# Kernel tuning notes

Hardware: AMD Instinct MI355X
Metric: run time of the kernel (lower is better)

The kernel has to match this reference:

```python
import jax, jax.numpy as jnp
import numpy as np
import math

# ---- hyperparameters (from __init__) ----
S = 64.0
M = 0.45
EASY_MARGIN = False
ALPHA = 0.0
BETA = 0.0
EPS_OT = 0.1   # self.eps
NITER = 6      # self.niter
COS_M = math.cos(M)
SIN_M = math.sin(M)
TH = math.cos(math.pi - M)
MM = math.sin(math.pi - M) * M

# ---- shapes ----
B = 24
D_EMB = 512
N_CLASSES = 10000
C_CH = 256   # channels -> number of OT points per image
H = 14       # spatial -> point dim H*H = 196


def setup_inputs() -> dict:
    key = jax.random.key(0)
    k1, k2, k3, k4 = jax.random.split(key, 4)
    embeddings = jax.random.normal(k1, (B, D_EMB), dtype=jnp.float32)
    conv_features = jax.random.normal(k2, (B, C_CH, H, H), dtype=jnp.float32)
    label = jax.random.randint(k3, (B,), 0, 8)
    # nn.init.normal_(kernel, std=0.01)
    kernel = jax.random.normal(k4, (D_EMB, N_CLASSES), dtype=jnp.float32) * 0.01
    return {"embeddings": embeddings, "conv_features": conv_features,
            "kernel": kernel, "label": label, "epoch": 1}


def _cdist(x, y):
    # Euclidean pairwise distance via GEMM: x (n,d), y (m,d) -> (n,m)
    x2 = jnp.sum(x * x, axis=-1)[:, None]
    y2 = jnp.sum(y * y, axis=-1)[None, :]
    d2 = jnp.maximum(x2 + y2 - 2.0 * (x @ y.T), 0.0)
    return jnp.sqrt(d2 + 1e-12)


def _sinkhorn_dist(x, y):
    # Entropic OT distance <T, C> with uniform marginals, log-domain Sinkhorn.
    C = _cdist(x, y)                       # (n, m)
    n, m = C.shape
    log_mu = -jnp.log(jnp.float32(n))
    log_nu = -jnp.log(jnp.float32(m))
    f = jnp.zeros((n,), C.dtype)
    g = jnp.zeros((m,), C.dtype)
    for _ in range(NITER):  # fixed 6 iterations
        f = -EPS_OT * jax.nn.logsumexp((g[None, :] - C) / EPS_OT + log_nu, axis=1)
        g = -EPS_OT * jax.nn.logsumexp((f[:, None] - C) / EPS_OT + log_mu, axis=0)
    T = jnp.exp((f[:, None] + g[None, :] - C) / EPS_OT + log_mu + log_nu)
    return jnp.sum(T * C)


def reference(embeddings, conv_features, kernel, label, epoch):
    b = embeddings.shape[0]
    emb = embeddings / jnp.linalg.norm(embeddings, axis=1, keepdims=True)
    kn = kernel / jnp.linalg.norm(kernel, axis=0, keepdims=True)
    cos_theta = jnp.clip(emb @ kn, -1.0, 1.0)          # (B, n_classes)
    origin_cos = cos_theta

    rows = jnp.arange(b)
    tl = cos_theta[rows, label]                         # target logit (B,)
    sin_t = jnp.sqrt(jnp.maximum(1.0 - tl * tl, 0.0))
    ctm = tl * COS_M - sin_t * SIN_M
    if EASY_MARGIN:
        ftl = jnp.where(tl > 0.0, ctm, tl)
    else:
        ftl = jnp.where(tl > TH, ctm, tl - MM)
    cos_theta = cos_theta.at[rows, label].set(ftl)
    arcfaceloss = cos_theta * S

    # ---- triplet mining on embedding cosine similarities ----
    dists = emb @ emb.T                                 # (B, B) cosine sims
    eq = label[:, None] == label[None, :]               # (B, B) same-class mask
    # diff_low[a,p,n] = cos(a,n) - cos(a,p)
    diff = dists[:, None, :] - dists[:, :, None]        # (a, p, n)
    valid = eq[:, :, None] & (~eq)[:, None, :] & (diff > -ALPHA)
    n_cosine_pair = jnp.sum(valid)

    if epoch >= 0:
        feats = conv_features.reshape(b, conv_features.shape[1], -1)  # (B, C, H*H)
        # batched Sinkhorn distance for all (a,b) image pairs: (B, B)
        D = jax.vmap(lambda xa: jax.vmap(lambda xb: _sinkhorn_dist(xa, xb))(feats))(feats)
        dis = jnp.maximum(D[:, :, None] - D[:, None, :], -BETA)       # (a, p, n)
        hit = valid & (dis > 0.0)
        ot_pair = jnp.sum(hit)
        wass = jnp.sum(jnp.where(hit, dis, 0.0))
        wass_loss = jnp.where(wass > 0.0,
                              wass / jnp.maximum(ot_pair, 1).astype(wass.dtype),
                              jnp.zeros((), wass.dtype))
    else:
        ot_pair = jnp.zeros((), jnp.int32)
        wass_loss = jnp.zeros(())

    return (arcfaceloss, wass_loss, origin_cos * S, n_cosine_pair, ot_pair)
```

## Files before the change

### kernel.cpp

```cpp
#include <hip/hip_runtime.h>
#include <math.h>

#define B_SZ 24
#define D_EMBD 512
#define N_CLS 10000
#define CC 256
#define HH 196
#define KPAD 224

#define NPAIR 276
#define NARC 40
#define NGRAM 36

#define S_SCALE 64.0f
#define COS_M 0.9004471023526769f
#define SIN_M 0.43496553411123023f
#define TH_C (-0.9004471023526769f)
#define MM_C 0.19573449035005357f
#define KSC 14.4269504088896f
#define C2E 0.0693147180559945f

typedef short bfrag8 __attribute__((ext_vector_type(8)));
typedef float facc4 __attribute__((ext_vector_type(4)));

#if __has_builtin(__builtin_amdgcn_exp2f)
#define EXP2F(x) __builtin_amdgcn_exp2f(x)
#else
#define EXP2F(x) exp2f(x)
#endif
#if __has_builtin(__builtin_amdgcn_logf)
#define LOG2F(x) __builtin_amdgcn_logf(x)
#else
#define LOG2F(x) __log2f(x)
#endif

__device__ inline unsigned short f2bf_rne(float x) {
    union { float f; unsigned u; } cv; cv.f = x;
    unsigned r = cv.u + 0x7FFFu + ((cv.u >> 16) & 1u);
    return (unsigned short)(r >> 16);
}
__device__ inline float bf2f(unsigned short h) {
    union { unsigned u; float f; } cv; cv.u = ((unsigned)h) << 16; return cv.f;
}

__global__ __launch_bounds__(1024) void k_pre(const float* __restrict__ conv,
        unsigned short* __restrict__ hiP, unsigned short* __restrict__ loP,
        float* __restrict__ nrm) {
    const int t = threadIdx.x;
    const int img = blockIdx.x;
    const int row = t >> 2, sch = t & 3;
    const float* src = conv + (img*CC + row)*HH;
    unsigned short* hb = hiP + (img*CC + row)*KPAD;
    unsigned short* lb = loP + (img*CC + row)*KPAD;
    float ps = 0.f;
    for (int c = sch; c < 28; c += 4) {
        const int k0 = c*8;
        float v[8];
        if (k0 + 8 <= HH) {
            const float4* s4 = (const float4*)(src + k0);
            float4 u0 = s4[0], u1 = s4[1];
            v[0]=u0.x; v[1]=u0.y; v[2]=u0.z; v[3]=u0.w;
            v[4]=u1.x; v[5]=u1.y; v[6]=u1.z; v[7]=u1.w;
        } else {
            #pragma unroll
            for (int j = 0; j < 8; ++j) v[j] = (k0 + j < HH) ? src[k0 + j] : 0.f;
        }
        union { unsigned short s[8]; bfrag8 v8; } uh, ul;
        #pragma unroll
        for (int j = 0; j < 8; ++j) {
            ps = fmaf(v[j], v[j], ps);
            unsigned short hbv = f2bf_rne(v[j]);
            uh.s[j] = hbv;
            ul.s[j] = f2bf_rne(v[j] - bf2f(hbv));
        }
        *(bfrag8*)(hb + k0) = uh.v8;
        *(bfrag8*)(lb + k0) = ul.v8;
    }
    ps += __shfl_xor(ps, 1, 64); ps += __shfl_xor(ps, 2, 64);
    if (sch == 0) nrm[img*CC + row] = ps;
}

__global__ __launch_bounds__(1024) void k_fused_pre(const float* __restrict__ emb,
        const float* __restrict__ kern, const int* __restrict__ label,
        const unsigned short* __restrict__ hiP, const unsigned short* __restrict__ loP,
        const float* __restrict__ nrm, float* __restrict__ dists,
        float* __restrict__ Dmat, float* __restrict__ out) {
    const int t = threadIdx.x;
    const int bid = blockIdx.x;

    __shared__ __align__(16) char smem[131072];

    if (bid >= NPAIR) {
        const int sb = bid - NPAIR;
        if (sb >= NARC) {
            const int gid = sb - NARC;
            int l = t & 63, w16 = t >> 6;
            if (gid == 0 && t < B_SZ) Dmat[t * B_SZ + t] = 0.f;
            int pid = gid * 16 + w16;
            if (pid >= B_SZ * B_SZ) return;
            int i = pid / B_SZ, j = pid - (pid / B_SZ) * B_SZ;
            float sij = 0.f, sii = 0.f, sjj = 0.f;
            #pragma unroll
            for (int u = 0; u < 8; ++u) {
                float vi = emb[i*D_EMBD + u*64 + l];
                float vj = emb[j*D_EMBD + u*64 + l];
                sij = fmaf(vi, vj, sij); sii = fmaf(vi, vi, sii); sjj = fmaf(vj, vj, sjj);
            }
            #pragma unroll
            for (int o = 1; o < 64; o <<= 1) {
                sij += __shfl_xor(sij, o, 64);
                sii += __shfl_xor(sii, o, 64);
                sjj += __shfl_xor(sjj, o, 64);
            }
            if (l == 0) dists[pid] = sij * rsqrtf(sii * sjj);
            return;
        }

        float* es = (float*)smem;
        float* inv_s = es + B_SZ * D_EMBD;
        int* lab_s = (int*)(inv_s + B_SZ);
        {
            const float4* s4 = (const float4*)emb;
            float4* d4 = (float4*)es;
            #pragma unroll
            for (int i = 0; i < 3; ++i) d4[i*1024 + t] = s4[i*1024 + t];
        }
        if (t < B_SZ) lab_s[t] = label[t];
        __syncthreads();
        {
            int l = t & 63, w = t >> 6;
            for (int r = w; r < B_SZ; r += 16) {
                float s = 0.f;
                #pragma unroll
                for (int u = 0; u < 8; ++u) { float v = es[r*D_EMBD + u*64 + l]; s = fmaf(v, v, s); }
                #pragma unroll
                for (int o = 1; o < 64; o <<= 1) s += __shfl_xor(s, o, 64);
                if (l == 0) inv_s[r] = rsqrtf(s);
            }
        }
        __syncthreads();

        const int cc = t >> 2, kc = t & 3;
        const int col = sb * 256 + cc;
        const int cL = col < N_CLS ? col : N_CLS - 1;
        float acc[B_SZ];
        #pragma unroll
        for (int r = 0; r < B_SZ; ++r) acc[r] = 0.f;
        float cn = 0.f;
        const int kb0 = kc << 7;
        for (int u = 0; u < 32; ++u) {
            const int um = (u + kc) & 31;
            const int kb = kb0 + (um << 2);
            float kv0 = kern[(kb+0)*N_CLS + cL];
            float kv1 = kern[(kb+1)*N_CLS + cL];
            float kv2 = kern[(kb+2)*N_CLS + cL];
            float kv3 = kern[(kb+3)*N_CLS + cL];
            cn = fmaf(kv0,kv0,cn); cn = fmaf(kv1,kv1,cn);
            cn = fmaf(kv2,kv2,cn); cn = fmaf(kv3,kv3,cn);
            #pragma unroll
            for (int r = 0; r < B_SZ; ++r) {
                const float4 e = *(const float4*)&es[r*D_EMBD + kb];
                acc[r] = fmaf(e.x, kv0, acc[r]);
                acc[r] = fmaf(e.y, kv1, acc[r]);
                acc[r] = fmaf(e.z, kv2, acc[r]);
                acc[r] = fmaf(e.w, kv3, acc[r]);
            }
        }
        cn += __shfl_xor(cn, 1, 64); cn += __shfl_xor(cn, 2, 64);
        #pragma unroll
        for (int r = 0; r < B_SZ; ++r) {
            acc[r] += __shfl_xor(acc[r], 1, 64);
            acc[r] += __shfl_xor(acc[r], 2, 64);
        }
        if (kc == 0 && col < N_CLS) {
            const float invk = rsqrtf(cn);
            #pragma unroll
            for (int r = 0; r < B_SZ; ++r) {
                float cosv = fminf(fmaxf(acc[r] * inv_s[r] * invk, -1.f), 1.f);
                float oc = cosv * S_SCALE;
                float af = oc;
                if (lab_s[r] == col) {
                    float tl = cosv;
                    float sint = sqrtf(fmaxf(1.f - tl*tl, 0.f));
                    float ctm = tl*COS_M - sint*SIN_M;
                    float ftl = (tl > TH_C) ? ctm : (tl - MM_C);
                    af = ftl * S_SCALE;
                }
                out[r*N_CLS + col] = af;
                out[240001 + r*N_CLS + col] = oc;
            }
        }
        return;
    }

    unsigned short* SB = (unsigned short*)smem;
    float* rowred = (float*)smem;
    float* colred = rowred + 1024;
    float* rm_l   = colred + 1024;
    float* z_l    = rm_l + 256;
    float* g_l    = z_l + 256;
    float* q_l    = g_l + 256;
    float* p_l    = q_l + 256;
    float* na_s   = p_l + 256;
    float* nb_s   = na_s + 256;
    float* wredF  = nb_s + 256;
    float* wredG  = wredF + 4;
    float* wredD  = wredG + 4;
    float* gsh    = wredD + 16;

    const int w = t >> 6;
    const int wr = w >> 2, wc = w & 3;
    const int q = (t >> 4) & 3, c0 = t & 15;
    const int R0 = wr * 64, C0 = wc * 64;

    int rem = bid, a = 0;
    while (rem >= 23 - a) { rem -= 23 - a; ++a; }
    int b = a + 1 + rem;

    const int sn = t >> 2;
    const int sch = t & 3;
    const unsigned short* gAh = hiP + (a*CC + sn)*KPAD + sch*8;
    const unsigned short* gAl = loP + (a*CC + sn)*KPAD + sch*8;
    const unsigned short* gBh = hiP + (b*CC + sn)*KPAD + sch*8;
    const unsigned short* gBl = loP + (b*CC + sn)*KPAD + sch*8;
    const int so = sn*32 + sch*8;

    facc4 acc[4][4];
    #pragma unroll
    for (int i = 0; i < 4; ++i)
        #pragma unroll
        for (int j = 0; j < 4; ++j) acc[i][j] = (facc4){0.f, 0.f, 0.f, 0.f};

    uint4 pAh, pAl, pBh, pBl;
    pAh = *(const uint4*)(gAh); pAl = *(const uint4*)(gAl);
    pBh = *(const uint4*)(gBh); pBl = *(const uint4*)(gBl);
    {
        unsigned short* base = SB;
        *(uint4*)(base + so)          = pAh;
        *(uint4*)(base + 8192 + so)   = pAl;
        *(uint4*)(base + 16384 + so)  = pBh;
        *(uint4*)(base + 24576 + so)  = pBl;
    }
    pAh = *(const uint4*)(gAh + 32); pAl = *(const uint4*)(gAl + 32);
    pBh = *(const uint4*)(gBh + 32); pBl = *(const uint4*)(gBl + 32);

    for (int s = 0; s < 7; ++s) {
        __syncthreads();
        if (s < 6) {
            unsigned short* base = SB + ((s + 1) & 1) * 32768;
            *(uint4*)(base + so)          = pAh;
            *(uint4*)(base + 8192 + so)   = pAl;
            *(uint4*)(base + 16384 + so)  = pBh;
            *(uint4*)(base + 24576 + so)  = pBl;
        }
        unsigned short* Ah = SB + (s & 1) * 32768;
        unsigned short* Al = Ah + 8192;
        unsigned short* Bh = Al + 8192;
        unsigned short* Bl = Bh + 8192;
        bfrag8 bh4[4], bl4[4];
        #pragma unroll
        for (int tj = 0; tj < 4; ++tj) {
            int col = C0 + tj*16 + c0;
            bh4[tj] = *(const bfrag8*)(Bh + col*32 + q*8);
            bl4[tj] = *(const bfrag8*)(Bl + col*32 + q*8);
        }
        #pragma unroll
        for (int ti = 0; ti < 4; ++ti) {
            int row = R0 + ti*16 + c0;
            bfrag8 ah = *(const bfrag8*)(Ah + row*32 + q*8);
            bfrag8 al = *(const bfrag8*)(Al + row*32 + q*8);
            #pragma unroll
            for (int tj = 0; tj < 4; ++tj) {
                acc[ti][tj] = __builtin_amdgcn_mfma_f32_16x16x32_bf16(ah, bh4[tj], acc[ti][tj], 0, 0, 0);
                acc[ti][tj] = __builtin_amdgcn_mfma_f32_16x16x32_bf16(ah, bl4[tj], acc[ti][tj], 0, 0, 0);
                acc[ti][tj] = __builtin_amdgcn_mfma_f32_16x16x32_bf16(al, bh4[tj], acc[ti][tj], 0, 0, 0);
            }
        }
        if (s < 5) {
            const int ko = (s + 2) * 32;
            pAh = *(const uint4*)(gAh + ko); pAl = *(const uint4*)(gAl + ko);
            pBh = *(const uint4*)(gBh + ko); pBl = *(const uint4*)(gBl + ko);
        }
    }
    __syncthreads();

    if (t < 256) {
        na_s[t] = nrm[a*CC + t];
        nb_s[t] = nrm[b*CC + t];
        p_l[t] = 1.f;
    }
    if (t < 4) { wredG[t] = 0.f; wredF[t] = 8.f; }
    if (t == 0) *gsh = 0.f;
    __syncthreads();

    facc4 E[4][4];
    {
        float nbv[4];
        #pragma unroll
        for (int tj = 0; tj < 4; ++tj) nbv[tj] = nb_s[C0 + tj*16 + c0];
        #pragma unroll
        for (int ti = 0; ti < 4; ++ti) {
            facc4 nav = *(const facc4*)&na_s[R0 + ti*16 + q*4];
            #pragma unroll
            for (int tj = 0; tj < 4; ++tj) {
                #pragma unroll
                for (int r = 0; r < 4; ++r) {
                    float d2 = fmaxf(nav[r] + nbv[tj] - 2.f*acc[ti][tj][r], 0.f);
                    E[ti][tj][r] = KSC * sqrtf(d2 + 1e-12f);
                }
            }
        }
    }

    const int istar = ((c0&1)<<3) | ((c0&2)<<1) | ((c0&4)>>1) | ((c0&8)>>3);
    const int rowstar = R0 + (istar>>2)*16 + q*4 + (istar&3);
    const int tjstar = ((q&1)<<1) | (q>>1);
    const int colstar = C0 + tjstar*16 + c0;

    {
        float v16[16];
        #pragma unroll
        for (int ti = 0; ti < 4; ++ti)
            #pragma unroll
            for (int r = 0; r < 4; ++r)
                v16[ti*4+r] = fminf(fminf(E[ti][0][r], E[ti][1][r]),
                                    fminf(E[ti][2][r], E[ti][3][r]));
        #pragma unroll
        for (int p = 0; p < 4; ++p) {
            const int m = 1 << p, hsz = 8 >> p;
            const bool hi = (c0 >> p) & 1;
            #pragma unroll
            for (int j = 0; j < hsz; ++j) {
                float mine = hi ? v16[j+hsz] : v16[j];
                float send = hi ? v16[j] : v16[j+hsz];
                v16[j] = fminf(mine, __shfl_xor(send, m, 64));
            }
        }
        rowred[wc*256 + rowstar] = v16[0];
    }
    __syncthreads();
    if (t < 256)
        rm_l[t] = fminf(fminf(rowred[t], rowred[256+t]), fminf(rowred[512+t], rowred[768+t]));
    __syncthreads();

    #pragma unroll
    for (int ti = 0; ti < 4; ++ti) {
        facc4 rmv = *(const facc4*)&rm_l[R0 + ti*16 + q*4];
        #pragma unroll
        for (int tj = 0; tj < 4; ++tj)
            #pragma unroll
            for (int r = 0; r < 4; ++r)
                E[ti][tj][r] = EXP2F(rmv[r] - E[ti][tj][r]);
    }

    #pragma unroll 1
    for (int it = 0; it < 6; ++it) {
        float Gstale = fmaxf(fmaxf(wredG[0], wredG[1]), fmaxf(wredG[2], wredG[3]));
        float MS     = fmaxf(fmaxf(wredF[0], wredF[1]), fmaxf(wredF[2], wredF[3]));
        float P4[4];
        #pragma unroll
        for (int tj = 0; tj < 4; ++tj) P4[tj] = p_l[C0 + tj*16 + c0];
        float v16[16];
        #pragma unroll
        for (int ti = 0; ti < 4; ++ti)
            #pragma unroll
            for (int r = 0; r < 4; ++r) {
                float s = 0.f;
                #pragma unroll
                for (int tj = 0; tj < 4; ++tj) s = fmaf(E[ti][tj][r], P4[tj], s);
                v16[ti*4+r] = s;
            }
        #pragma unroll
        for (int p = 0; p < 4; ++p) {
            const int m = 1 << p, hsz = 8 >> p;
            const bool hi = (c0 >> p) & 1;
            #pragma unroll
            for (int j = 0; j < hsz; ++j) {
                float mine = hi ? v16[j+hsz] : v16[j];
                float send = hi ? v16[j] : v16[j+hsz];
                v16[j] = mine + __shfl_xor(send, m, 64);
            }
        }
        rowred[wc*256 + rowstar] = v16[0];
        __syncthreads();
        if (t < 256) {
            float GS = *gsh;
            float s = rowred[t] + rowred[256+t] + rowred[512+t] + rowred[768+t];
            float z = 8.f - GS - LOG2F(s);
            z_l[t] = z;
            q_l[t] = EXP2F(z - MS);
            float m = z;
            #pragma unroll
            for (int o = 1; o < 64; o <<= 1) m = fmaxf(m, __shfl_xor(m, o, 64));
            if ((t & 63) == 0) wredF[t >> 6] = m;
        }
        __syncthreads();
        float Q[16];
        #pragma unroll
        for (int ti = 0; ti < 4; ++ti) {
            facc4 qv = *(const facc4*)&q_l[R0 + ti*16 + q*4];
            #pragma unroll
            for (int r = 0; r < 4; ++r) Q[ti*4+r] = qv[r];
        }
        float w4[4];
        #pragma unroll
        for (int tj = 0; tj < 4; ++tj) {
            float s = 0.f;
            #pragma unroll
            for (int ti = 0; ti < 4; ++ti)
                #pragma unroll
                for (int r = 0; r < 4; ++r) s = fmaf(E[ti][tj][r], Q[ti*4+r], s);
            w4[tj] = s;
        }
        #pragma unroll
        for (int p = 0; p < 2; ++p) {
            const int m = 16 << p, hsz = 2 >> p;
            const bool hi = (q >> p) & 1;
            #pragma unroll
            for (int j = 0; j < hsz; ++j) {
                float mine = hi ? w4[j+hsz] : w4[j];
                float send = hi ? w4[j] : w4[j+hsz];
                w4[j] = mine + __shfl_xor(send, m, 64);
            }
        }
        colred[wr*256 + colstar] = w4[0];
        __syncthreads();
        if (t < 256) {
            float s = colred[t] + colred[256+t] + colred[512+t] + colred[768+t];
            float G = 8.f - MS - LOG2F(s);
            g_l[t] = G;
            p_l[t] = EXP2F(G - Gstale);
            float m = G;
            #pragma unroll
            for (int o = 1; o < 64; o <<= 1) m = fmaxf(m, __shfl_xor(m, o, 64));
            if ((t & 63) == 0) wredG[t >> 6] = m;
            if (t == 0) *gsh = Gstale;
        }
        __syncthreads();
    }

    {
        float G4[4];
        #pragma unroll
        for (int tj = 0; tj < 4; ++tj) G4[tj] = g_l[C0 + tj*16 + c0] - 16.f;
        float d = 0.f;
        #pragma unroll
        for (int ti = 0; ti < 4; ++ti) {
            facc4 zv = *(const facc4*)&z_l[R0 + ti*16 + q*4];
            facc4 rmv = *(const facc4*)&rm_l[R0 + ti*16 + q*4];
            #pragma unroll
            for (int tj = 0; tj < 4; ++tj) {
                #pragma unroll
                for (int r = 0; r < 4; ++r) {
                    float e = fmaxf(E[ti][tj][r], 1e-45f);
                    float lE = LOG2F(e);
                    float ce = rmv[r] - lE;
                    d = fmaf(EXP2F(zv[r] + G4[tj] + lE), ce, d);
                }
            }
        }
        d *= C2E;
        #pragma unroll
        for (int o = 1; o < 64; o <<= 1) d += __shfl_xor(d, o, 64);
        if ((t & 63) == 0) wredD[w] = d;
        __syncthreads();
        if (t == 0) {
            float s = 0.f;
            #pragma unroll
            for (int i = 0; i < 16; ++i) s += wredD[i];
            Dmat[a*B_SZ + b] = s;
            Dmat[b*B_SZ + a] = s;
        }
    }
}

__global__ __launch_bounds__(1024) void k_fused_loc(const float* __restrict__ emb,
        const float* __restrict__ conv, const float* __restrict__ kern,
        const int* __restrict__ label, float* __restrict__ dists,
        float* __restrict__ Dmat, float* __restrict__ out) {
    const int t = threadIdx.x;
    const int bid = blockIdx.x;

    __shared__ __align__(16) char smem[65536];

    if (bid >= NPAIR) {
        const int sb = bid - NPAIR;
        if (sb >= NARC) {
            const int gid = sb - NARC;
            int l = t & 63, w16 = t >> 6;
            if (gid == 0 && t < B_SZ) Dmat[t * B_SZ + t] = 0.f;
            int pid = gid * 16 + w16;
            if (pid >= B_SZ * B_SZ) return;
            int i = pid / B_SZ, j = pid - (pid / B_SZ) * B_SZ;
            float sij = 0.f, sii = 0.f, sjj = 0.f;
            #pragma unroll
            for (int u = 0; u < 8; ++u) {
                float vi = emb[i*D_EMBD + u*64 + l];
                float vj = emb[j*D_EMBD + u*64 + l];
                sij = fmaf(vi, vj, sij); sii = fmaf(vi, vi, sii); sjj = fmaf(vj, vj, sjj);
            }
            #pragma unroll
            for (int o = 1; o < 64; o <<= 1) {
                sij += __shfl_xor(sij, o, 64);
                sii += __shfl_xor(sii, o, 64);
                sjj += __shfl_xor(sjj, o, 64);
            }
            if (l == 0) dists[pid] = sij * rsqrtf(sii * sjj);
            return;
        }

        float* es = (float*)smem;
        float* inv_s = es + B_SZ * D_EMBD;
        int* lab_s = (int*)(inv_s + B_SZ);
        {
            const float4* s4 = (const float4*)emb;
            float4* d4 = (float4*)es;
            #pragma unroll
            for (int i = 0; i < 3; ++i) d4[i*1024 + t] = s4[i*1024 + t];
        }
        if (t < B_SZ) lab_s[t] = label[t];
        __syncthreads();
        {
            int l = t & 63, w = t >> 6;
            for (int r = w; r < B_SZ; r += 16) {
                float s = 0.f;
                #pragma unroll
                for (int u = 0; u < 8; ++u) { float v = es[r*D_EMBD + u*64 + l]; s = fmaf(v, v, s); }
                #pragma unroll
                for (int o = 1; o < 64; o <<= 1) s += __shfl_xor(s, o, 64);
                if (l == 0) inv_s[r] = rsqrtf(s);
            }
        }
        __syncthreads();

        const int cc = t >> 2, kc = t & 3;
        const int col = sb * 256 + cc;
        const int cL = col < N_CLS ? col : N_CLS - 1;
        float acc[B_SZ];
        #pragma unroll
        for (int r = 0; r < B_SZ; ++r) acc[r] = 0.f;
        float cn = 0.f;
        const int kb0 = kc << 7;
        for (int u = 0; u < 32; ++u) {
            const int um = (u + kc) & 31;
            const int kb = kb0 + (um << 2);
            float kv0 = kern[(kb+0)*N_CLS + cL];
            float kv1 = kern[(kb+1)*N_CLS + cL];
            float kv2 = kern[(kb+2)*N_CLS + cL];
            float kv3 = kern[(kb+3)*N_CLS + cL];
            cn = fmaf(kv0,kv0,cn); cn = fmaf(kv1,kv1,cn);
            cn = fmaf(kv2,kv2,cn); cn = fmaf(kv3,kv3,cn);
            #pragma unroll
            for (int r = 0; r < B_SZ; ++r) {
                const float4 e = *(const float4*)&es[r*D_EMBD + kb];
                acc[r] = fmaf(e.x, kv0, acc[r]);
                acc[r] = fmaf(e.y, kv1, acc[r]);
                acc[r] = fmaf(e.z, kv2, acc[r]);
                acc[r] = fmaf(e.w, kv3, acc[r]);
            }
        }
        cn += __shfl_xor(cn, 1, 64); cn += __shfl_xor(cn, 2, 64);
        #pragma unroll
        for (int r = 0; r < B_SZ; ++r) {
            acc[r] += __shfl_xor(acc[r], 1, 64);
            acc[r] += __shfl_xor(acc[r], 2, 64);
        }
        if (kc == 0 && col < N_CLS) {
            const float invk = rsqrtf(cn);
            #pragma unroll
            for (int r = 0; r < B_SZ; ++r) {
                float cosv = fminf(fmaxf(acc[r] * inv_s[r] * invk, -1.f), 1.f);
                float oc = cosv * S_SCALE;
                float af = oc;
                if (lab_s[r] == col) {
                    float tl = cosv;
                    float sint = sqrtf(fmaxf(1.f - tl*tl, 0.f));
                    float ctm = tl*COS_M - sint*SIN_M;
                    float ftl = (tl > TH_C) ? ctm : (tl - MM_C);
                    af = ftl * S_SCALE;
                }
                out[r*N_CLS + col] = af;
                out[240001 + r*N_CLS + col] = oc;
            }
        }
        return;
    }

    unsigned short* Ah = (unsigned short*)smem;
    unsigned short* Al = Ah + 8192;
    unsigned short* Bh = Al + 8192;
    unsigned short* Bl = Bh + 8192;
    float* rowred = (float*)smem;
    float* colred = rowred + 1024;
    float* rm_l   = colred + 1024;
    float* z_l    = rm_l + 256;
    float* g_l    = z_l + 256;
    float* q_l    = g_l + 256;
    float* p_l    = q_l + 256;
    float* na_s   = p_l + 256;
    float* nb_s   = na_s + 256;
    float* wredF  = nb_s + 256;
    float* wredG  = wredF + 4;
    float* wredD  = wredG + 4;
    float* gsh    = wredD + 16;

    const int w = t >> 6;
    const int wr = w >> 2, wc = w & 3;
    const int q = (t >> 4) & 3, c0 = t & 15;
    const int R0 = wr * 64, C0 = wc * 64;

    int rem = bid, a = 0;
    while (rem >= 23 - a) { rem -= 23 - a; ++a; }
    int b = a + 1 + rem;
    const float* xa = conv + a*CC*HH;
    const float* xb = conv + b*CC*HH;

    const int sn = t >> 2;
    const int sch = t & 3;

    facc4 acc[4][4];
    #pragma unroll
    for (int i = 0; i < 4; ++i)
        #pragma unroll
        for (int j = 0; j < 4; ++j) acc[i][j] = (facc4){0.f, 0.f, 0.f, 0.f};

    float pa = 0.f, pb = 0.f;

    for (int ks = 0; ks < 224; ks += 32) {
        __syncthreads();
        #pragma unroll
        for (int p = 0; p < 2; ++p) {
            int k0 = ks + sch*8;
            const float* src = (p ? xb : xa) + sn*HH + k0;
            float v[8];
            if (k0 + 8 <= HH) {
                const float4* s4 = (const float4*)src;
                float4 u0 = s4[0], u1 = s4[1];
                v[0]=u0.x; v[1]=u0.y; v[2]=u0.z; v[3]=u0.w;
                v[4]=u1.x; v[5]=u1.y; v[6]=u1.z; v[7]=u1.w;
            } else {
                #pragma unroll
                for (int j = 0; j < 8; ++j) v[j] = (k0 + j < HH) ? src[j] : 0.f;
            }
            float ps = 0.f;
            union { unsigned short s[8]; bfrag8 v8; } uh, ul;
            #pragma unroll
            for (int j = 0; j < 8; ++j) {
                ps = fmaf(v[j], v[j], ps);
                unsigned short hb = f2bf_rne(v[j]);
                uh.s[j] = hb;
                ul.s[j] = f2bf_rne(v[j] - bf2f(hb));
            }
            if (p) pb += ps; else pa += ps;
            unsigned short* dh = (p ? Bh : Ah) + sn*32 + sch*8;
            unsigned short* dl = (p ? Bl : Al) + sn*32 + sch*8;
            *(bfrag8*)dh = uh.v8;
            *(bfrag8*)dl = ul.v8;
        }
        __syncthreads();
        bfrag8 bh4[4], bl4[4];
        #pragma unroll
        for (int tj = 0; tj < 4; ++tj) {
            int col = C0 + tj*16 + c0;
            bh4[tj] = *(const bfrag8*)(Bh + col*32 + q*8);
            bl4[tj] = *(const bfrag8*)(Bl + col*32 + q*8);
        }
        #pragma unroll
        for (int ti = 0; ti < 4; ++ti) {
            int row = R0 + ti*16 + c0;
            bfrag8 ah = *(const bfrag8*)(Ah + row*32 + q*8);
            bfrag8 al = *(const bfrag8*)(Al + row*32 + q*8);
            #pragma unroll
            for (int tj = 0; tj < 4; ++tj) {
                acc[ti][tj] = __builtin_amdgcn_mfma_f32_16x16x32_bf16(ah, bh4[tj], acc[ti][tj], 0, 0, 0);
                acc[ti][tj] = __builtin_amdgcn_mfma_f32_16x16x32_bf16(ah, bl4[tj], acc[ti][tj], 0, 0, 0);
                acc[ti][tj] = __builtin_amdgcn_mfma_f32_16x16x32_bf16(al, bh4[tj], acc[ti][tj], 0, 0, 0);
            }
        }
    }
    __syncthreads();

    pa += __shfl_xor(pa, 1, 64); pa += __shfl_xor(pa, 2, 64);
    pb += __shfl_xor(pb, 1, 64); pb += __shfl_xor(pb, 2, 64);
    if (sch == 0) { na_s[sn] = pa; nb_s[sn] = pb; }
    if (t < 256) p_l[t] = 1.f;
    if (t < 4) { wredG[t] = 0.f; wredF[t] = 8.f; }
    if (t == 0) *gsh = 0.f;
    __syncthreads();

    facc4 E[4][4];
    {
        float nbv[4];
        #pragma unroll
        for (int tj = 0; tj < 4; ++tj) nbv[tj] = nb_s[C0 + tj*16 + c0];
        #pragma unroll
        for (int ti = 0; ti < 4; ++ti) {
            facc4 nav = *(const facc4*)&na_s[R0 + ti*16 + q*4];
            #pragma unroll
            for (int tj = 0; tj < 4; ++tj) {
                #pragma unroll
                for (int r = 0; r < 4; ++r) {
                    float d2 = fmaxf(nav[r] + nbv[tj] - 2.f*acc[ti][tj][r], 0.f);
                    E[ti][tj][r] = KSC * sqrtf(d2 + 1e-12f);
                }
            }
        }
    }

    const int istar = ((c0&1)<<3) | ((c0&2)<<1) | ((c0&4)>>1) | ((c0&8)>>3);
    const int rowstar = R0 + (istar>>2)*16 + q*4 + (istar&3);
    const int tjstar = ((q&1)<<1) | (q>>1);
    const int colstar = C0 + tjstar*16 + c0;

    {
        float v16[16];
        #pragma unroll
        for (int ti = 0; ti < 4; ++ti)
            #pragma unroll
            for (int r = 0; r < 4; ++r)
                v16[ti*4+r] = fminf(fminf(E[ti][0][r], E[ti][1][r]),
                                    fminf(E[ti][2][r], E[ti][3][r]));
        #pragma unroll
        for (int p = 0; p < 4; ++p) {
            const int m = 1 << p, hsz = 8 >> p;
            const bool hi = (c0 >> p) & 1;
            #pragma unroll
            for (int j = 0; j < hsz; ++j) {
                float mine = hi ? v16[j+hsz] : v16[j];
                float send = hi ? v16[j] : v16[j+hsz];
                v16[j] = fminf(mine, __shfl_xor(send, m, 64));
            }
        }
        rowred[wc*256 + rowstar] = v16[0];
    }
    __syncthreads();
    if (t < 256)
        rm_l[t] = fminf(fminf(rowred[t], rowred[256+t]), fminf(rowred[512+t], rowred[768+t]));
    __syncthreads();

    #pragma unroll
    for (int ti = 0; ti < 4; ++ti) {
        facc4 rmv = *(const facc4*)&rm_l[R0 + ti*16 + q*4];
        #pragma unroll
        for (int tj = 0; tj < 4; ++tj)
            #pragma unroll
            for (int r = 0; r < 4; ++r)
                E[ti][tj][r] = EXP2F(rmv[r] - E[ti][tj][r]);
    }

    #pragma unroll 1
    for (int it = 0; it < 6; ++it) {
        float Gstale = fmaxf(fmaxf(wredG[0], wredG[1]), fmaxf(wredG[2], wredG[3]));
        float MS     = fmaxf(fmaxf(wredF[0], wredF[1]), fmaxf(wredF[2], wredF[3]));
        float P4[4];
        #pragma unroll
        for (int tj = 0; tj < 4; ++tj) P4[tj] = p_l[C0 + tj*16 + c0];
        float v16[16];
        #pragma unroll
        for (int ti = 0; ti < 4; ++ti)
            #pragma unroll
            for (int r = 0; r < 4; ++r) {
                float s = 0.f;
                #pragma unroll
                for (int tj = 0; tj < 4; ++tj) s = fmaf(E[ti][tj][r], P4[tj], s);
                v16[ti*4+r] = s;
            }
        #pragma unroll
        for (int p = 0; p < 4; ++p) {
            const int m = 1 << p, hsz = 8 >> p;
            const bool hi = (c0 >> p) & 1;
            #pragma unroll
            for (int j = 0; j < hsz; ++j) {
                float mine = hi ? v16[j+hsz] : v16[j];
                float send = hi ? v16[j] : v16[j+hsz];
                v16[j] = mine + __shfl_xor(send, m, 64);
            }
        }
        rowred[wc*256 + rowstar] = v16[0];
        __syncthreads();
        if (t < 256) {
            float GS = *gsh;
            float s = rowred[t] + rowred[256+t] + rowred[512+t] + rowred[768+t];
            float z = 8.f - GS - LOG2F(s);
            z_l[t] = z;
            q_l[t] = EXP2F(z - MS);
            float m = z;
            #pragma unroll
            for (int o = 1; o < 64; o <<= 1) m = fmaxf(m, __shfl_xor(m, o, 64));
            if ((t & 63) == 0) wredF[t >> 6] = m;
        }
        __syncthreads();
        float Q[16];
        #pragma unroll
        for (int ti = 0; ti < 4; ++ti) {
            facc4 qv = *(const facc4*)&q_l[R0 + ti*16 + q*4];
            #pragma unroll
            for (int r = 0; r < 4; ++r) Q[ti*4+r] = qv[r];
        }
        float w4[4];
        #pragma unroll
        for (int tj = 0; tj < 4; ++tj) {
            float s = 0.f;
            #pragma unroll
            for (int ti = 0; ti < 4; ++ti)
                #pragma unroll
                for (int r = 0; r < 4; ++r) s = fmaf(E[ti][tj][r], Q[ti*4+r], s);
            w4[tj] = s;
        }
        #pragma unroll
        for (int p = 0; p < 2; ++p) {
            const int m = 16 << p, hsz = 2 >> p;
            const bool hi = (q >> p) & 1;
            #pragma unroll
            for (int j = 0; j < hsz; ++j) {
                float mine = hi ? w4[j+hsz] : w4[j];
                float send = hi ? w4[j] : w4[j+hsz];
                w4[j] = mine + __shfl_xor(send, m, 64);
            }
        }
        colred[wr*256 + colstar] = w4[0];
        __syncthreads();
        if (t < 256) {
            float s = colred[t] + colred[256+t] + colred[512+t] + colred[768+t];
            float G = 8.f - MS - LOG2F(s);
            g_l[t] = G;
            p_l[t] = EXP2F(G - Gstale);
            float m = G;
            #pragma unroll
            for (int o = 1; o < 64; o <<= 1) m = fmaxf(m, __shfl_xor(m, o, 64));
            if ((t & 63) == 0) wredG[t >> 6] = m;
            if (t == 0) *gsh = Gstale;
        }
        __syncthreads();
    }

    {
        float G4[4];
        #pragma unroll
        for (int tj = 0; tj < 4; ++tj) G4[tj] = g_l[C0 + tj*16 + c0] - 16.f;
        float d = 0.f;
        #pragma unroll
        for (int ti = 0; ti < 4; ++ti) {
            facc4 zv = *(const facc4*)&z_l[R0 + ti*16 + q*4];
            facc4 rmv = *(const facc4*)&rm_l[R0 + ti*16 + q*4];
            #pragma unroll
            for (int tj = 0; tj < 4; ++tj) {
                #pragma unroll
                for (int r = 0; r < 4; ++r) {
                    float e = fmaxf(E[ti][tj][r], 1e-45f);
                    float lE = LOG2F(e);
                    float ce = rmv[r] - lE;
                    d = fmaf(EXP2F(zv[r] + G4[tj] + lE), ce, d);
                }
            }
        }
        d *= C2E;
        #pragma unroll
        for (int o = 1; o < 64; o <<= 1) d += __shfl_xor(d, o, 64);
        if ((t & 63) == 0) wredD[w] = d;
        __syncthreads();
        if (t == 0) {
            float s = 0.f;
            #pragma unroll
            for (int i = 0; i < 16; ++i) s += wredD[i];
            Dmat[a*B_SZ + b] = s;
            Dmat[b*B_SZ + a] = s;
        }
    }
}

__global__ __launch_bounds__(256) void k_fin(const int* __restrict__ label,
        const float* __restrict__ dists, const float* __restrict__ Dmat,
        float* __restrict__ out) {
    const int t = threadIdx.x;
    __shared__ float ds[576], Dm[576];
    __shared__ int lab[B_SZ];
    __shared__ float wls[4]; __shared__ int wnp[4], wot[4];
    for (int i = t; i < 576; i += 256) { ds[i] = dists[i]; Dm[i] = Dmat[i]; }
    if (t < B_SZ) lab[t] = label[t];
    __syncthreads();
    int np = 0, ot = 0; float wsum = 0.f;
    for (int idx = t; idx < 24*24*24; idx += 256) {
        int a2 = idx / 576;
        int rest = idx - a2*576;
        int p2 = rest / 24;
        int n2 = rest - p2*24;
        int la = lab[a2];
        if (la == lab[p2] && la != lab[n2]) {
            float diff = ds[a2*24 + n2] - ds[a2*24 + p2];
            if (diff > 0.f) {
                ++np;
                float dd = Dm[a2*24 + p2] - Dm[a2*24 + n2];
                if (dd > 0.f) { ++ot; wsum += dd; }
            }
        }
    }
    #pragma unroll
    for (int o = 1; o < 64; o <<= 1) {
        np += __shfl_xor(np, o, 64);
        ot += __shfl_xor(ot, o, 64);
        wsum += __shfl_xor(wsum, o, 64);
    }
    int w = t >> 6;
    if ((t & 63) == 0) { wnp[w] = np; wot[w] = ot; wls[w] = wsum; }
    __syncthreads();
    if (t == 0) {
        int tnp = wnp[0]+wnp[1]+wnp[2]+wnp[3];
        int tot = wot[0]+wot[1]+wot[2]+wot[3];
        float tws = wls[0]+wls[1]+wls[2]+wls[3];
        int den = tot > 1 ? tot : 1;
        float wl = (tws > 0.f) ? tws / (float)den : 0.f;
        out[240000] = wl;
        out[480001] = (float)tnp;
        out[480002] = (float)tot;
    }
}

extern "C" void kernel_launch(void* const* d_in, const int* in_sizes, int n_in,
                              void* d_out, int out_size, void* d_ws, size_t ws_size,
                              hipStream_t stream) {
    (void)in_sizes; (void)n_in; (void)out_size;
    const float* emb  = (const float*)d_in[0];
    const float* conv = (const float*)d_in[1];
    const float* kern = (const float*)d_in[2];
    const int*   lab  = (const int*)d_in[3];
    float* out = (float*)d_out;
    float* ws  = (float*)d_ws;
    float* dists = ws;
    float* Dmat  = ws + 576;

    const size_t NEED = 7296u * 4u + 2u * (size_t)(24 * CC * KPAD) * 2u;

    if (ws_size >= NEED) {
        float* nrm = ws + 1152;
        unsigned short* hiP = (unsigned short*)(ws + 7296);
        unsigned short* loP = hiP + 24*CC*KPAD;
        k_pre<<<24, 1024, 0, stream>>>(conv, hiP, loP, nrm);
        k_fused_pre<<<NPAIR + NARC + NGRAM, 1024, 0, stream>>>(emb, kern, lab, hiP, loP, nrm,
                                                               dists, Dmat, out);
    } else {
        k_fused_loc<<<NPAIR + NARC + NGRAM, 1024, 0, stream>>>(emb, conv, kern, lab,
                                                               dists, Dmat, out);
    }
    k_fin<<<1, 256, 0, stream>>>(lab, dists, Dmat, out);
}
```

Measured before the change: 191.4 us.

## Load GEMM tiles directly to LDS and widen preprocessing grid

```diff
diff --git a/kernel.cpp b/kernel.cpp
--- a/kernel.cpp
+++ b/kernel.cpp
@@ -34,6 +34,10 @@
 #define LOG2F(x) __log2f(x)
 #endif
 
+#define GL16(gp, lp) __builtin_amdgcn_global_load_lds( \
+    (const __attribute__((address_space(1))) unsigned int*)(gp), \
+    (__attribute__((address_space(3))) unsigned int*)(lp), 16, 0, 0)
+
 __device__ inline unsigned short f2bf_rne(float x) {
     union { float f; unsigned u; } cv; cv.f = x;
     unsigned r = cv.u + 0x7FFFu + ((cv.u >> 16) & 1u);
@@ -47,14 +51,13 @@
         unsigned short* __restrict__ hiP, unsigned short* __restrict__ loP,
         float* __restrict__ nrm) {
     const int t = threadIdx.x;
-    const int img = blockIdx.x;
-    const int row = t >> 2, sch = t & 3;
+    const int img = blockIdx.x >> 3;
+    const int row = (blockIdx.x & 7) * 32 + (t >> 5);
+    const int c = t & 31;
     const float* src = conv + (img*CC + row)*HH;
-    unsigned short* hb = hiP + (img*CC + row)*KPAD;
-    unsigned short* lb = loP + (img*CC + row)*KPAD;
     float ps = 0.f;
-    for (int c = sch; c < 28; c += 4) {
-        const int k0 = c*8;
+    if (c < 28) {
+        const int k0 = c * 8;
         float v[8];
         if (k0 + 8 <= HH) {
             const float4* s4 = (const float4*)(src + k0);
@@ -73,11 +76,12 @@
             uh.s[j] = hbv;
             ul.s[j] = f2bf_rne(v[j] - bf2f(hbv));
         }
-        *(bfrag8*)(hb + k0) = uh.v8;
-        *(bfrag8*)(lb + k0) = ul.v8;
-    }
-    ps += __shfl_xor(ps, 1, 64); ps += __shfl_xor(ps, 2, 64);
-    if (sch == 0) nrm[img*CC + row] = ps;
+        *(bfrag8*)(hiP + (img*CC + row)*KPAD + k0) = uh.v8;
+        *(bfrag8*)(loP + (img*CC + row)*KPAD + k0) = ul.v8;
+    }
+    #pragma unroll
+    for (int o = 1; o < 32; o <<= 1) ps += __shfl_xor(ps, o, 64);
+    if ((t & 31) == 0) nrm[img*CC + row] = ps;
 }
 
 __global__ __launch_bounds__(1024) void k_fused_pre(const float* __restrict__ emb,
@@ -223,7 +227,6 @@
     const unsigned short* gAl = loP + (a*CC + sn)*KPAD + sch*8;
     const unsigned short* gBh = hiP + (b*CC + sn)*KPAD + sch*8;
     const unsigned short* gBl = loP + (b*CC + sn)*KPAD + sch*8;
-    const int so = sn*32 + sch*8;
 
     facc4 acc[4][4];
     #pragma unroll
@@ -231,27 +234,20 @@
         #pragma unroll
         for (int j = 0; j < 4; ++j) acc[i][j] = (facc4){0.f, 0.f, 0.f, 0.f};
 
-    uint4 pAh, pAl, pBh, pBl;
-    pAh = *(const uint4*)(gAh); pAl = *(const uint4*)(gAl);
-    pBh = *(const uint4*)(gBh); pBl = *(const uint4*)(gBl);
-    {
-        unsigned short* base = SB;
-        *(uint4*)(base + so)          = pAh;
-        *(uint4*)(base + 8192 + so)   = pAl;
-        *(uint4*)(base + 16384 + so)  = pBh;
-        *(uint4*)(base + 24576 + so)  = pBl;
-    }
-    pAh = *(const uint4*)(gAh + 32); pAl = *(const uint4*)(gAl + 32);
-    pBh = *(const uint4*)(gBh + 32); pBl = *(const uint4*)(gBl + 32);
+    GL16(gAh, SB + t*8);
+    GL16(gAl, SB + 8192 + t*8);
+    GL16(gBh, SB + 16384 + t*8);
+    GL16(gBl, SB + 24576 + t*8);
+    __syncthreads();
 
     for (int s = 0; s < 7; ++s) {
-        __syncthreads();
         if (s < 6) {
+            const int ko = (s + 1) * 32;
             unsigned short* base = SB + ((s + 1) & 1) * 32768;
-            *(uint4*)(base + so)          = pAh;
-            *(uint4*)(base + 8192 + so)   = pAl;
-            *(uint4*)(base + 16384 + so)  = pBh;
-            *(uint4*)(base + 24576 + so)  = pBl;
+            GL16(gAh + ko, base + t*8);
+            GL16(gAl + ko, base + 8192 + t*8);
+            GL16(gBh + ko, base + 16384 + t*8);
+            GL16(gBl + ko, base + 24576 + t*8);
         }
         unsigned short* Ah = SB + (s & 1) * 32768;
         unsigned short* Al = Ah + 8192;
@@ -276,13 +272,8 @@
                 acc[ti][tj] = __builtin_amdgcn_mfma_f32_16x16x32_bf16(al, bh4[tj], acc[ti][tj], 0, 0, 0);
             }
         }
-        if (s < 5) {
-            const int ko = (s + 2) * 32;
-            pAh = *(const uint4*)(gAh + ko); pAl = *(const uint4*)(gAl + ko);
-            pBh = *(const uint4*)(gBh + ko); pBl = *(const uint4*)(gBl + ko);
-        }
-    }
-    __syncthreads();
+        __syncthreads();
+    }
 
     if (t < 256) {
         na_s[t] = nrm[a*CC + t];
@@ -935,7 +926,7 @@
         float* nrm = ws + 1152;
         unsigned short* hiP = (unsigned short*)(ws + 7296);
         unsigned short* loP = hiP + 24*CC*KPAD;
-        k_pre<<<24, 1024, 0, stream>>>(conv, hiP, loP, nrm);
+        k_pre<<<192, 1024, 0, stream>>>(conv, hiP, loP, nrm);
         k_fused_pre<<<NPAIR + NARC + NGRAM, 1024, 0, stream>>>(emb, kern, lab, hiP, loP, nrm,
                                                                dists, Dmat, out);
     } else {
```

New measurement: 185.9 us. 1.03x faster.
